# Kernel tuning notes

Hardware: AMD Instinct MI355X
Metric: run time of the kernel (lower is better)

The kernel has to match this reference:

```python
import jax, jax.numpy as jnp
import numpy as np

D_MODEL = 1024
EXPAND = 2
D_INNER = D_MODEL * EXPAND  # 2048
D_STATE = 16
DT_RANK = 64
CONV_K = 4
LN_EPS = 1e-5
B_SZ, SEQ = 2, 2048


def setup_inputs() -> dict:
    key = jax.random.key(0)
    ks = jax.random.split(key, 10)
    x = jax.random.normal(ks[0], (B_SZ, SEQ, D_MODEL), dtype=jnp.float32)
    ln_g = jnp.ones((D_MODEL,), jnp.float32)
    ln_b = jnp.zeros((D_MODEL,), jnp.float32)
    W_in = jax.random.normal(ks[1], (2 * D_INNER, D_MODEL), jnp.float32) * 0.02
    conv_w = jax.random.normal(ks[2], (D_INNER, 1, CONV_K), jnp.float32) * 0.2
    conv_b = jnp.zeros((D_INNER,), jnp.float32)
    # A_log = log(repeat(arange(1..d_state), d_inner))
    A_log = jnp.log(jnp.broadcast_to(jnp.arange(1, D_STATE + 1, dtype=jnp.float32), (D_INNER, D_STATE)))
    D_param = jnp.ones((D_INNER,), jnp.float32)
    x_proj_w = jax.random.normal(ks[3], (DT_RANK + 2 * D_STATE, D_INNER), jnp.float32) * 0.02
    dt_std = DT_RANK ** -0.5
    dt_w = jax.random.uniform(ks[4], (D_INNER, DT_RANK), jnp.float32, -dt_std, dt_std)
    dt = jnp.exp(jax.random.uniform(ks[5], (D_INNER,), jnp.float32) * (np.log(0.1) - np.log(0.001)) + np.log(0.001))
    dt_b = dt + jnp.log(-jnp.expm1(-dt))  # inverse softplus
    W_out = jax.random.normal(ks[6], (D_MODEL, D_INNER), jnp.float32) * 0.02
    return dict(x=x, ln_g=ln_g, ln_b=ln_b, W_in=W_in, conv_w=conv_w, conv_b=conv_b,
                A_log=A_log, D_param=D_param, x_proj_w=x_proj_w, dt_w=dt_w, dt_b=dt_b, W_out=W_out)


def _selective_scan(u, delta, A, B, C):
    # u, delta: (b,l,d); A: (d,n); B, C: (b,l,n)
    deltaA = jnp.exp(delta[..., None] * A[None, None])          # (b,l,d,n)
    dBu = delta[..., None] * B[:, :, None, :] * u[..., None]    # (b,l,d,n)

    def step(s, inp):
        dA_t, dBu_t, C_t = inp          # (b,d,n), (b,d,n), (b,n)
        s = dA_t * s + dBu_t
        y = jnp.einsum('bdn,bn->bd', s, C_t)
        return s, y

    s0 = jnp.zeros((u.shape[0], u.shape[2], A.shape[1]), u.dtype)
    xs = (jnp.moveaxis(deltaA, 1, 0), jnp.moveaxis(dBu, 1, 0), jnp.moveaxis(C, 1, 0))
    _, ys = jax.lax.scan(step, s0, xs)
    return jnp.moveaxis(ys, 0, 1)       # (b,l,d)


def reference(x, ln_g, ln_b, W_in, conv_w, conv_b, A_log, D_param, x_proj_w, dt_w, dt_b, W_out):
    residual = x
    mu = jnp.mean(x, -1, keepdims=True)
    var = jnp.var(x, -1, keepdims=True)
    xn = (x - mu) * jax.lax.rsqrt(var + LN_EPS) * ln_g + ln_b
    xz = xn @ W_in.T                               # (b,l,2*d_inner)
    xc, z = jnp.split(xz, 2, axis=-1)
    # causal depthwise conv1d (left-pad k-1)
    lhs = jnp.swapaxes(xc, 1, 2)                   # (b,d,l)
    conv = jax.lax.conv_general_dilated(
        lhs, conv_w, window_strides=(1,), padding=[(CONV_K - 1, 0)],
        dimension_numbers=('NCH', 'OIH', 'NCH'), feature_group_count=D_INNER)
    conv = conv + conv_b[None, :, None]
    xc = jax.nn.silu(jnp.swapaxes(conv, 1, 2))     # (b,l,d)
    # selective SSM
    x_dbl = xc @ x_proj_w.T
    delta_r, B, C = jnp.split(x_dbl, [DT_RANK, DT_RANK + D_STATE], axis=-1)
    delta = jax.nn.softplus(delta_r @ dt_w.T + dt_b)
    A = -jnp.exp(A_log)
    y = _selective_scan(xc, delta, A, B, C)
    y = y + xc * D_param
    y = y * jax.nn.silu(z)
    out = y @ W_out.T
    return out + residual
```

## Files before the change

### kernel.cpp

```cpp
#include <hip/hip_runtime.h>
#include <hip/hip_bf16.h>
#include <math.h>

typedef __hip_bfloat16 bf16;

#define D_MODEL 1024
#define D_INNER 2048
#define NTOK    4096
#define SEQ     2048
#define BSZ     2
#define DSTATE  16
#define DTRANK  64
#define NCH     64
#define CHLEN   32
#define NPAIR   4096
#define XDS     128

__device__ __forceinline__ float b2f(bf16 v) { return __bfloat162float(v); }
__device__ __forceinline__ bf16  f2b(float v) { return __float2bfloat16(v); }
__device__ __forceinline__ short f2bs(float v) {
    bf16 h = __float2bfloat16(v);
    short s; __builtin_memcpy(&s, &h, 2); return s;
}

typedef __attribute__((ext_vector_type(8))) short short8;
typedef __attribute__((ext_vector_type(4))) float f32x4;

__device__ __forceinline__ void async_copy16(const void* g, void* l) {
    __builtin_amdgcn_global_load_lds(
        (const __attribute__((address_space(1))) unsigned int*)g,
        (__attribute__((address_space(3))) unsigned int*)l,
        16, 0, 0);
}

__global__ void k_prep(const float* __restrict__ x, const float* __restrict__ g,
                       const float* __restrict__ b, bf16* __restrict__ xn,
                       const float* __restrict__ W_in, short* __restrict__ wInb,
                       const float* __restrict__ xpw, short* __restrict__ xpwb,
                       const float* __restrict__ dtw, short* __restrict__ dtwb,
                       float* __restrict__ xdbl) {
    int bid = blockIdx.x;
    int tid = threadIdx.x;
    if (bid < 4096) {
        int t = bid;
        const float* row = x + (size_t)t * D_MODEL;
        float v[4];
        float s = 0.f, q = 0.f;
#pragma unroll
        for (int i = 0; i < 4; ++i) {
            int idx = tid + i * 256;
            v[i] = row[idx];
            s += v[i]; q += v[i] * v[i];
        }
        __shared__ float sh_s[256], sh_q[256];
        sh_s[tid] = s; sh_q[tid] = q;
        __syncthreads();
        for (int o = 128; o > 0; o >>= 1) {
            if (tid < o) { sh_s[tid] += sh_s[tid + o]; sh_q[tid] += sh_q[tid + o]; }
            __syncthreads();
        }
        float mu  = sh_s[0] * (1.f / D_MODEL);
        float var = sh_q[0] * (1.f / D_MODEL) - mu * mu;
        float rs  = rsqrtf(var + 1e-5f);
#pragma unroll
        for (int i = 0; i < 4; ++i) {
            int idx = tid + i * 256;
            float o = (v[i] - mu) * rs * g[idx] + b[idx];
            xn[(size_t)t * D_MODEL + idx] = f2b(o);
        }
    } else if (bid < 8192) {
        int i = (bid - 4096) * 256 + tid;
        float4 v = reinterpret_cast<const float4*>(W_in)[i];
        short4 o;
        o.x = f2bs(v.x); o.y = f2bs(v.y); o.z = f2bs(v.z); o.w = f2bs(v.w);
        reinterpret_cast<short4*>(wInb)[i] = o;
    } else if (bid < 8448) {
        int i = (bid - 8192) * 256 + tid;
        int row = i >> 9;
        short4 o;
        if (row < 96) {
            float4 v = reinterpret_cast<const float4*>(xpw)[i];
            o.x = f2bs(v.x); o.y = f2bs(v.y); o.z = f2bs(v.z); o.w = f2bs(v.w);
        } else { o.x = o.y = o.z = o.w = 0; }
        reinterpret_cast<short4*>(xpwb)[i] = o;
    } else if (bid < 8576) {
        int i = (bid - 8448) * 256 + tid;
        float4 v = reinterpret_cast<const float4*>(dtw)[i];
        short4 o;
        o.x = f2bs(v.x); o.y = f2bs(v.y); o.z = f2bs(v.z); o.w = f2bs(v.w);
        reinterpret_cast<short4*>(dtwb)[i] = o;
    } else {
        int i = (bid - 8576) * 256 + tid;
        reinterpret_cast<float4*>(xdbl)[i] = (float4){0.f, 0.f, 0.f, 0.f};
    }
}

__global__ void k_f2b(const float* __restrict__ in, short* __restrict__ out) {
    int i = blockIdx.x * 256 + threadIdx.x;
    float4 v = reinterpret_cast<const float4*>(in)[i];
    short4 o;
    o.x = f2bs(v.x); o.y = f2bs(v.y); o.z = f2bs(v.z); o.w = f2bs(v.w);
    reinterpret_cast<short4*>(out)[i] = o;
}

__global__ void k_extract_dr(const float* __restrict__ xdbl, short* __restrict__ drb) {
    int i = blockIdx.x * 256 + threadIdx.x;
    int t = i >> 4;
    int jg = (i & 15) * 4;
    float4 v = *reinterpret_cast<const float4*>(&xdbl[(size_t)t * XDS + jg]);
    short4 o;
    o.x = f2bs(v.x); o.y = f2bs(v.y); o.z = f2bs(v.z); o.w = f2bs(v.w);
    *reinterpret_cast<short4*>(&drb[(size_t)t * DTRANK + jg]) = o;
}

#define GBK 32
template<int NT>
__global__ __launch_bounds__(256) void k_gemm_mfma(
    const short* __restrict__ A, const short* __restrict__ Bw,
    int N, int K, int mode,
    float* __restrict__ Cf, bf16* __restrict__ Cz,
    const float* __restrict__ res, float* __restrict__ Cout,
    const float* __restrict__ bias)
{
    constexpr int ABUF = 128 * GBK;
    constexpr int BBUF = NT * GBK;
    constexpr int AF   = (NT == 128) ? 4 : 2;
    __shared__ short As[2 * ABUF];
    __shared__ short Bs[2 * BBUF];
    const int tid  = threadIdx.x;
    const int lane = tid & 63;
    const int wave = tid >> 6;
    const int rowbase = (NT == 128) ? (wave >> 1) * 64 : wave * 32;
    const int colbase = (NT == 128) ? (wave & 1) * 64 : 0;
    const int m0 = blockIdx.y * 128;
    const int n0 = blockIdx.x * NT;
    const int lm = lane & 15;
    const int koff = (((lane >> 4) ^ ((lane >> 1) & 3)) * 8);

    const int srow = tid >> 2;
    const int skc  = (((tid & 3) ^ ((tid >> 3) & 3)) * 8);
    const size_t a_off0 = (size_t)(m0 + srow) * K + skc;
    const size_t a_off1 = (size_t)(m0 + srow + 64) * K + skc;
    const size_t b_off0 = (size_t)(n0 + srow) * K + skc;
    size_t b_off1 = 0;
    if constexpr (NT == 128) b_off1 = (size_t)(n0 + srow + 64) * K + skc;

    f32x4 acc[AF][4];
#pragma unroll
    for (int i = 0; i < AF; ++i)
#pragma unroll
        for (int j = 0; j < 4; ++j)
            acc[i][j] = (f32x4){0.f, 0.f, 0.f, 0.f};

    const int kchunk = K / gridDim.z;
    const int kbeg = blockIdx.z * kchunk;
    const int kend = kbeg + kchunk;

    {
        char* aD = (char*)As + tid * 16;
        char* bD = (char*)Bs + tid * 16;
        async_copy16(A + a_off0 + kbeg, aD);
        async_copy16(A + a_off1 + kbeg, aD + 4096);
        async_copy16(Bw + b_off0 + kbeg, bD);
        if constexpr (NT == 128) async_copy16(Bw + b_off1 + kbeg, bD + 4096);
    }

    int cur = 0;
    for (int k0 = kbeg; k0 < kend; k0 += GBK) {
        __syncthreads();
        int k1 = k0 + GBK;
        if (k1 < kend) {
            int nxt = cur ^ 1;
            char* aD = (char*)As + nxt * (ABUF * 2) + tid * 16;
            char* bD = (char*)Bs + nxt * (BBUF * 2) + tid * 16;
            async_copy16(A + a_off0 + k1, aD);
            async_copy16(A + a_off1 + k1, aD + 4096);
            async_copy16(Bw + b_off0 + k1, bD);
            if constexpr (NT == 128) async_copy16(Bw + b_off1 + k1, bD + 4096);
        }

        const short* Ab = As + cur * ABUF;
        const short* Bb = Bs + cur * BBUF;
        short8 af[AF], bf[4];
#pragma unroll
        for (int t = 0; t < AF; ++t)
            af[t] = *reinterpret_cast<const short8*>(&Ab[(rowbase + t * 16 + lm) * GBK + koff]);
#pragma unroll
        for (int t = 0; t < 4; ++t)
            bf[t] = *reinterpret_cast<const short8*>(&Bb[(colbase + t * 16 + lm) * GBK + koff]);
#pragma unroll
        for (int tm = 0; tm < AF; ++tm)
#pragma unroll
            for (int tn = 0; tn < 4; ++tn)
                acc[tm][tn] = __builtin_amdgcn_mfma_f32_16x16x32_bf16(
                    af[tm], bf[tn], acc[tm][tn], 0, 0, 0);
        cur ^= 1;
    }

    const int rq = (lane >> 4) * 4;
#pragma unroll
    for (int tm = 0; tm < AF; ++tm) {
#pragma unroll
        for (int tn = 0; tn < 4; ++tn) {
            f32x4 v = acc[tm][tn];
            int col = n0 + colbase + tn * 16 + lm;
#pragma unroll
            for (int r = 0; r < 4; ++r) {
                int row = m0 + rowbase + tm * 16 + rq + r;
                float val = v[r];
                if (mode == 0) {
                    if (col < D_INNER) Cf[(size_t)row * D_INNER + col] = val;
                    else               Cz[(size_t)row * D_INNER + (col - D_INNER)] = f2b(val);
                } else if (mode == 1) {
                    Cout[(size_t)row * N + col] = val + res[(size_t)row * N + col];
                } else if (mode == 2) {
                    atomicAdd(&Cf[(size_t)row * N + col], val);
                } else if (mode == 3) {
                    float a = val + bias[col];
                    float sp = (a > 20.f) ? a : log1pf(expf(a));
                    Cf[(size_t)row * N + col] = sp;
                } else {
                    Cf[(size_t)blockIdx.z * 4096 * N + (size_t)row * N + col] = val;
                }
            }
        }
    }
}

template<int BM>
__global__ __launch_bounds__(512, 2) void k_gemm8(
    const short* __restrict__ A, const short* __restrict__ Bw,
    int N, int K, int mode,
    float* __restrict__ Cf, bf16* __restrict__ Cz)
{
    constexpr int WM    = BM / 2;
    constexpr int MQ    = WM / 32;
    constexpr int ATILE = BM * 64;
    constexpr int ABYT  = BM * 128;
    constexpr int BREG  = BM * 256;
    __shared__ short lds[2 * ATILE + 2 * 16384];
    char* ldsc = (char*)lds;
    const int tid  = threadIdx.x;
    const int lane = tid & 63;
    const int wave = tid >> 6;
    const int wr   = wave >> 2;
    const int wc   = wave & 3;
    const int lm   = lane & 15;
    const int q4   = lane >> 4;

    const int gx = gridDim.x;
    int n2 = blockIdx.y * gx + blockIdx.x;
    const int nwg = gx * gridDim.y;
    n2 = (n2 & 7) * (nwg >> 3) + (n2 >> 3);
    const int m0 = (n2 / gx) * BM;
    const int n0 = (n2 % gx) * 256;

    const int r0  = tid >> 3;
    const int ksw = ((tid & 7) ^ (r0 & 7)) << 3;

    const int NTt   = K / 64 / gridDim.z;
    const int kbase = blockIdx.z * NTt;

    const short* gA = A  + (size_t)(m0 + r0) * K + ksw;
    const short* gB = Bw + (size_t)(n0 + r0) * K + ksw;

#define STAGE_A8(h, kt, bb) do {                                             \
        const short* s_ = gA + (size_t)(h) * 128 * K + (size_t)(kt) * 64;    \
        char* d_ = ldsc + (bb) * ABYT + (h) * 16384 + tid * 16;              \
        async_copy16(s_, d_);                                                \
        async_copy16(s_ + (size_t)64 * K, d_ + 8192);                        \
    } while (0)
#define STAGE_B8(h, kt, bb) do {                                             \
        const short* s_ = gB + (size_t)(h) * 128 * K + (size_t)(kt) * 64;    \
        char* d_ = ldsc + BREG + (bb) * 32768 + (h) * 16384 + tid * 16;      \
        async_copy16(s_, d_);                                                \
        async_copy16(s_ + (size_t)64 * K, d_ + 8192);                        \
    } while (0)

    f32x4 acc[2][2][MQ][2];
#pragma unroll
    for (int a = 0; a < 2; ++a)
#pragma unroll
        for (int c = 0; c < 2; ++c)
#pragma unroll
            for (int t = 0; t < MQ; ++t)
#pragma unroll
                for (int u = 0; u < 2; ++u)
                    acc[a][c][t][u] = (f32x4){0.f, 0.f, 0.f, 0.f};

    STAGE_B8(0, kbase + 0, 0); STAGE_B8(1, kbase + 0, 0);
    STAGE_A8(0, kbase + 0, 0);
    if constexpr (BM == 256) STAGE_A8(1, kbase + 0, 0);
    STAGE_B8(0, kbase + 1, 1); STAGE_B8(1, kbase + 1, 1);
    asm volatile("s_waitcnt vmcnt(4)" ::: "memory");
    __builtin_amdgcn_s_barrier();

    short8 af[MQ][2], bf0[2][2], bf1[2][2];

    for (int tt = 0; tt < NTt; ++tt) {
        const int b  = tt & 1;
        const int bn = b ^ 1;
        const short* lA = lds + b * ATILE + wr * (WM * 64);
        const short* lB = lds + BM * 128 + b * 16384 + (wc >> 1) * 8192;
        const bool stA = (tt + 1 < NTt);
        const bool stB = (tt + 2 < NTt);

#pragma unroll
        for (int t = 0; t < MQ; ++t) {
            const int rr = t * 16 + lm;
            const int x8 = rr & 7;
            af[t][0] = *reinterpret_cast<const short8*>(&lA[rr * 64 + ((q4 ^ x8) << 3)]);
            af[t][1] = *reinterpret_cast<const short8*>(&lA[rr * 64 + (((4 + q4) ^ x8) << 3)]);
        }
#pragma unroll
        for (int t = 0; t < 2; ++t) {
            const int rr = (wc & 1) * 64 + t * 16 + lm;
            const int x8 = rr & 7;
            bf0[t][0] = *reinterpret_cast<const short8*>(&lB[rr * 64 + ((q4 ^ x8) << 3)]);
            bf0[t][1] = *reinterpret_cast<const short8*>(&lB[rr * 64 + (((4 + q4) ^ x8) << 3)]);
        }
        if (stA) STAGE_A8(0, kbase + tt + 1, bn);
        __builtin_amdgcn_s_barrier();
        asm volatile("s_waitcnt lgkmcnt(0)" ::: "memory");
        __builtin_amdgcn_s_setprio(1);
#pragma unroll
        for (int t = 0; t < MQ; ++t)
#pragma unroll
            for (int u = 0; u < 2; ++u) {
                acc[0][0][t][u] = __builtin_amdgcn_mfma_f32_16x16x32_bf16(af[t][0], bf0[u][0], acc[0][0][t][u], 0, 0, 0);
                acc[0][0][t][u] = __builtin_amdgcn_mfma_f32_16x16x32_bf16(af[t][1], bf0[u][1], acc[0][0][t][u], 0, 0, 0);
            }
        __builtin_amdgcn_s_setprio(0);
        __builtin_amdgcn_s_barrier();

#pragma unroll
        for (int t = 0; t < 2; ++t) {
            const int rr = (wc & 1) * 64 + 32 + t * 16 + lm;
            const int x8 = rr & 7;
            bf1[t][0] = *reinterpret_cast<const short8*>(&lB[rr * 64 + ((q4 ^ x8) << 3)]);
            bf1[t][1] = *reinterpret_cast<const short8*>(&lB[rr * 64 + (((4 + q4) ^ x8) << 3)]);
        }
        if constexpr (BM == 256) { if (stA) STAGE_A8(1, kbase + tt + 1, bn); }
        __builtin_amdgcn_s_barrier();
        asm volatile("s_waitcnt lgkmcnt(0)" ::: "memory");
        __builtin_amdgcn_s_setprio(1);
#pragma unroll
        for (int t = 0; t < MQ; ++t)
#pragma unroll
            for (int u = 0; u < 2; ++u) {
                acc[0][1][t][u] = __builtin_amdgcn_mfma_f32_16x16x32_bf16(af[t][0], bf1[u][0], acc[0][1][t][u], 0, 0, 0);
                acc[0][1][t][u] = __builtin_amdgcn_mfma_f32_16x16x32_bf16(af[t][1], bf1[u][1], acc[0][1][t][u], 0, 0, 0);
            }
        __builtin_amdgcn_s_setprio(0);
        __builtin_amdgcn_s_barrier();

#pragma unroll
        for (int t = 0; t < MQ; ++t) {
            const int rr = MQ * 16 + t * 16 + lm;
            const int x8 = rr & 7;
            af[t][0] = *reinterpret_cast<const short8*>(&lA[rr * 64 + ((q4 ^ x8) << 3)]);
            af[t][1] = *reinterpret_cast<const short8*>(&lA[rr * 64 + (((4 + q4) ^ x8) << 3)]);
        }
        if (stB) STAGE_B8(0, kbase + tt + 2, b);
        __builtin_amdgcn_s_barrier();
        asm volatile("s_waitcnt lgkmcnt(0)" ::: "memory");
        __builtin_amdgcn_s_setprio(1);
#pragma unroll
        for (int t = 0; t < MQ; ++t)
#pragma unroll
            for (int u = 0; u < 2; ++u) {
                acc[1][1][t][u] = __builtin_amdgcn_mfma_f32_16x16x32_bf16(af[t][0], bf1[u][0], acc[1][1][t][u], 0, 0, 0);
                acc[1][1][t][u] = __builtin_amdgcn_mfma_f32_16x16x32_bf16(af[t][1], bf1[u][1], acc[1][1][t][u], 0, 0, 0);
            }
        __builtin_amdgcn_s_setprio(0);
        __builtin_amdgcn_s_barrier();

        if (stB) {
            STAGE_B8(1, kbase + tt + 2, b);
            asm volatile("s_waitcnt vmcnt(4)" ::: "memory");
        } else if (stA) {
            asm volatile("s_waitcnt vmcnt(0)" ::: "memory");
        }
        __builtin_amdgcn_s_barrier();
        __builtin_amdgcn_s_setprio(1);
#pragma unroll
        for (int t = 0; t < MQ; ++t)
#pragma unroll
            for (int u = 0; u < 2; ++u) {
                acc[1][0][t][u] = __builtin_amdgcn_mfma_f32_16x16x32_bf16(af[t][0], bf0[u][0], acc[1][0][t][u], 0, 0, 0);
                acc[1][0][t][u] = __builtin_amdgcn_mfma_f32_16x16x32_bf16(af[t][1], bf0[u][1], acc[1][0][t][u], 0, 0, 0);
            }
        __builtin_amdgcn_s_setprio(0);
        __builtin_amdgcn_s_barrier();
    }
#undef STAGE_A8
#undef STAGE_B8

    const int rq = (lane >> 4) * 4;
#pragma unroll
    for (int qr = 0; qr < 2; ++qr)
#pragma unroll
    for (int qc = 0; qc < 2; ++qc)
#pragma unroll
    for (int t = 0; t < MQ; ++t)
#pragma unroll
    for (int u = 0; u < 2; ++u) {
        f32x4 v = acc[qr][qc][t][u];
        const int col = n0 + wc * 64 + qc * 32 + u * 16 + lm;
#pragma unroll
        for (int r = 0; r < 4; ++r) {
            const int row = m0 + wr * WM + qr * (WM / 2) + t * 16 + rq + r;
            if (mode == 0) {
                if (col < D_INNER) Cf[(size_t)row * D_INNER + col] = v[r];
                else               Cz[(size_t)row * D_INNER + (col - D_INNER)] = f2b(v[r]);
            } else {
                Cf[(size_t)blockIdx.z * 4096 * N + (size_t)row * N + col] = v[r];
            }
        }
    }
}

__global__ void k_reduce_out(const float* __restrict__ x, const float* __restrict__ P,
                             float* __restrict__ out) {
    int i = blockIdx.x * 256 + threadIdx.x;
    float4 a = reinterpret_cast<const float4*>(x)[i];
    float4 p = reinterpret_cast<const float4*>(P)[i];
    float4 q = reinterpret_cast<const float4*>(P + (size_t)4096 * 1024)[i];
    float4 o;
    o.x = a.x + p.x + q.x; o.y = a.y + p.y + q.y;
    o.z = a.z + p.z + q.z; o.w = a.w + p.w + q.w;
    reinterpret_cast<float4*>(out)[i] = o;
}

__global__ void k_conv(const float* __restrict__ xc, const float* __restrict__ cw,
                       const float* __restrict__ cb, bf16* __restrict__ xcs) {
    size_t idx = (size_t)blockIdx.x * blockDim.x + threadIdx.x;
    int d = (int)(idx & (D_INNER - 1));
    int l = (int)((idx >> 11) & (SEQ - 1));
    float w0 = cw[d * 4 + 0], w1 = cw[d * 4 + 1];
    float w2 = cw[d * 4 + 2], w3 = cw[d * 4 + 3];
    const float* base = xc + idx;
    float acc = cb[d] + w3 * base[0];
    if (l >= 1) acc += w2 * base[-(int)D_INNER];
    if (l >= 2) acc += w1 * base[-2 * (int)D_INNER];
    if (l >= 3) acc += w0 * base[-3 * (int)D_INNER];
    xcs[idx] = f2b(acc / (1.f + __expf(-acc)));
}

__global__ __launch_bounds__(256) void k_scan_partialB(
    const float* __restrict__ delta, const bf16* __restrict__ xcs,
    const float* __restrict__ xdbl, const float* __restrict__ A_log,
    bf16* __restrict__ chs, float* __restrict__ sumdl)
{
    __shared__ float Bsh[CHLEN][16];
    const int tid = threadIdx.x;
    const int d = blockIdx.x * 256 + tid;
    const int chunk = blockIdx.y;
    const int b = blockIdx.z;
    const size_t tbase = (size_t)b * SEQ + (size_t)chunk * CHLEN;

    if (tid < 128) {
        int t = tid >> 2, j = (tid & 3) * 4;
        float4 v = *reinterpret_cast<const float4*>(&xdbl[(tbase + t) * XDS + 64 + j]);
        *reinterpret_cast<float4*>(&Bsh[t][j]) = v;
    }
    float An[16];
#pragma unroll
    for (int j = 0; j < 4; ++j) {
        float4 v = *reinterpret_cast<const float4*>(&A_log[(size_t)d * DSTATE + j * 4]);
        An[j * 4 + 0] = -__expf(v.x); An[j * 4 + 1] = -__expf(v.y);
        An[j * 4 + 2] = -__expf(v.z); An[j * 4 + 3] = -__expf(v.w);
    }
    __syncthreads();

    float s[16];
#pragma unroll
    for (int n = 0; n < 16; ++n) s[n] = 0.f;
    float sd = 0.f;
    for (int t = 0; t < CHLEN; ++t) {
        size_t gt = tbase + t;
        float dl = delta[gt * D_INNER + d];
        float u  = b2f(xcs[gt * D_INNER + d]);
        float dlu = dl * u;
        sd += dl;
#pragma unroll
        for (int n = 0; n < 16; ++n) {
            float dA = __expf(dl * An[n]);
            s[n] = fmaf(dA, s[n], dlu * Bsh[t][n]);
        }
    }
    const int pair = b * D_INNER + d;
    bf16* co = chs + ((size_t)pair * NCH + chunk) * DSTATE;
#pragma unroll
    for (int n = 0; n < 16; ++n) co[n] = f2b(s[n]);
    sumdl[(size_t)pair * NCH + chunk] = sd;
}

__global__ void k_scan_combineB(const bf16* __restrict__ chs, const float* __restrict__ sumdl,
                                const float* __restrict__ A_log, bf16* __restrict__ sst) {
    int idx = blockIdx.x * 256 + threadIdx.x;
    int pair = idx >> 4;
    int n = idx & 15;
    int d = pair & (D_INNER - 1);
    float An = -__expf(A_log[(size_t)d * DSTATE + n]);
    float s = 0.f;
    for (int c = 0; c < NCH; ++c) {
        size_t o = ((size_t)pair * NCH + c) * DSTATE + n;
        float loc = b2f(chs[o]);
        float ap = __expf(An * sumdl[(size_t)pair * NCH + c]);
        sst[o] = f2b(s);
        s = fmaf(ap, s, loc);
    }
}

__global__ __launch_bounds__(256) void k_scan_finalB(
    const float* __restrict__ delta, const bf16* __restrict__ xcs,
    const float* __restrict__ xdbl, const bf16* __restrict__ zbuf,
    const float* __restrict__ A_log, const float* __restrict__ Dp,
    const bf16* __restrict__ sst, bf16* __restrict__ yf)
{
    __shared__ float BC[CHLEN][32];
    const int tid = threadIdx.x;
    const int d = blockIdx.x * 256 + tid;
    const int chunk = blockIdx.y;
    const int b = blockIdx.z;
    const size_t tbase = (size_t)b * SEQ + (size_t)chunk * CHLEN;

    {
        int t = tid >> 3, j = (tid & 7) * 4;
        float4 v = *reinterpret_cast<const float4*>(&xdbl[(tbase + t) * XDS + 64 + j]);
        *reinterpret_cast<float4*>(&BC[t][j]) = v;
    }
    float An[16];
#pragma unroll
    for (int j = 0; j < 4; ++j) {
        float4 v = *reinterpret_cast<const float4*>(&A_log[(size_t)d * DSTATE + j * 4]);
        An[j * 4 + 0] = -__expf(v.x); An[j * 4 + 1] = -__expf(v.y);
        An[j * 4 + 2] = -__expf(v.z); An[j * 4 + 3] = -__expf(v.w);
    }
    const int pair = b * D_INNER + d;
    float s[16];
    const bf16* so = sst + ((size_t)pair * NCH + chunk) * DSTATE;
#pragma unroll
    for (int n = 0; n < 16; ++n) s[n] = b2f(so[n]);
    const float Dv = Dp[d];
    __syncthreads();

    for (int t = 0; t < CHLEN; ++t) {
        size_t gt = tbase + t;
        float dl = delta[gt * D_INNER + d];
        float u  = b2f(xcs[gt * D_INNER + d]);
        float dlu = dl * u;
        float y = 0.f;
#pragma unroll
        for (int n = 0; n < 16; ++n) {
            float dA = __expf(dl * An[n]);
            s[n] = fmaf(dA, s[n], dlu * BC[t][n]);
            y = fmaf(s[n], BC[t][16 + n], y);
        }
        float zv = b2f(zbuf[gt * D_INNER + d]);
        float sz = zv / (1.f + __expf(-zv));
        yf[gt * D_INNER + d] = f2b((y + u * Dv) * sz);
    }
}

extern "C" void kernel_launch(void* const* d_in, const int* in_sizes, int n_in,
                              void* d_out, int out_size, void* d_ws, size_t ws_size,
                              hipStream_t stream) {
    const float* x      = (const float*)d_in[0];
    const float* ln_g   = (const float*)d_in[1];
    const float* ln_b   = (const float*)d_in[2];
    const float* W_in   = (const float*)d_in[3];
    const float* conv_w = (const float*)d_in[4];
    const float* conv_b = (const float*)d_in[5];
    const float* A_log  = (const float*)d_in[6];
    const float* D_par  = (const float*)d_in[7];
    const float* xpw    = (const float*)d_in[8];
    const float* dtw    = (const float*)d_in[9];
    const float* dtb    = (const float*)d_in[10];
    const float* W_out  = (const float*)d_in[11];
    float* out = (float*)d_out;

    char* ws = (char*)d_ws;
    bf16*  xn    = (bf16*)(ws + 0);
    bf16*  chs   = (bf16*)(ws + 0);
    bf16*  sst   = chs;
    short* wOutb = (short*)(ws + 0);
    float* xc    = (float*)(ws + 8388608);
    float* delta = xc;
    float* P0    = (float*)(ws + 8388608);
    bf16*  z     = (bf16*)(ws + 41943040);
    bf16*  yf    = z;
    short* wInb  = (short*)(ws + 58720256);
    bf16*  xcs   = (bf16*)(ws + 58720256);
    float* xdbl  = (float*)(ws + 75497472);
    float* sumdl = (float*)(ws + 77594624);
    short* drb   = (short*)(ws + 78643200);
    short* dtwb  = (short*)(ws + 79167488);
    short* xpwb  = (short*)(ws + 79429632);

    k_prep<<<9088, 256, 0, stream>>>(x, ln_g, ln_b, xn, W_in, wInb, xpw, xpwb, dtw, dtwb, xdbl);
    k_gemm8<256><<<dim3(4096 / 256, 4096 / 256, 1), 512, 0, stream>>>(
        (const short*)xn, wInb, 2 * D_INNER, D_MODEL, 0, xc, z);
    k_conv<<<(NTOK * D_INNER) / 256, 256, 0, stream>>>(xc, conv_w, conv_b, xcs);
    k_gemm_mfma<64><<<dim3(2, 32, 8), 256, 0, stream>>>(
        (const short*)xcs, xpwb, XDS, D_INNER, 2, xdbl, nullptr, nullptr, nullptr, nullptr);
    k_extract_dr<<<(NTOK * DTRANK / 4) / 256, 256, 0, stream>>>(xdbl, drb);
    k_gemm_mfma<64><<<dim3(D_INNER / 64, 32, 1), 256, 0, stream>>>(
        drb, dtwb, D_INNER, DTRANK, 3, delta, nullptr, nullptr, nullptr, dtb);
    k_scan_partialB<<<dim3(D_INNER / 256, NCH, BSZ), 256, 0, stream>>>(
        delta, xcs, xdbl, A_log, chs, sumdl);
    k_scan_combineB<<<(NPAIR * DSTATE) / 256, 256, 0, stream>>>(chs, sumdl, A_log, sst);
    k_scan_finalB<<<dim3(D_INNER / 256, NCH, BSZ), 256, 0, stream>>>(
        delta, xcs, xdbl, z, A_log, D_par, sst, yf);
    k_f2b<<<(D_MODEL * D_INNER / 4) / 256, 256, 0, stream>>>(W_out, wOutb);
    k_gemm8<128><<<dim3(D_MODEL / 256, 4096 / 128, 2), 512, 0, stream>>>(
        (const short*)yf, wOutb, D_MODEL, D_INNER, 4, P0, nullptr);
    k_reduce_out<<<(NTOK * D_MODEL / 4) / 256, 256, 0, stream>>>(x, P0, out);
}
```

Measured before the change: 363.2 us.

## Replace atomic split-K x_proj with partial buffers plus reduction; restructure gemm8 pipeline

The x_proj split-K GEMM now writes eight per-slice partial buffers (mode 4) instead of accumulating into a zeroed xdbl. A new reduction kernel sums the slices and writes both the bf16 dt-rank input and the fp32 B/C columns, which removes the zeroing pass in k_prep and the separate extract kernel. Separately, the 8-wave GEMM main loop is reordered: A and B global-to-LDS stages are issued at the start of each half-iteration, MFMA blocks are merged, and several barriers and lgkmcnt waits are dropped, with sched_barrier added to pin the ordering. Fewer barriers raise the risk of LDS read/write races and add extra traffic for the partial buffers.

```diff
diff --git a/kernel.cpp b/kernel.cpp
--- a/kernel.cpp
+++ b/kernel.cpp
@@ -37,8 +37,7 @@
                        const float* __restrict__ b, bf16* __restrict__ xn,
                        const float* __restrict__ W_in, short* __restrict__ wInb,
                        const float* __restrict__ xpw, short* __restrict__ xpwb,
-                       const float* __restrict__ dtw, short* __restrict__ dtwb,
-                       float* __restrict__ xdbl) {
+                       const float* __restrict__ dtw, short* __restrict__ dtwb) {
     int bid = blockIdx.x;
     int tid = threadIdx.x;
     if (bid < 4096) {
@@ -83,15 +82,12 @@
             o.x = f2bs(v.x); o.y = f2bs(v.y); o.z = f2bs(v.z); o.w = f2bs(v.w);
         } else { o.x = o.y = o.z = o.w = 0; }
         reinterpret_cast<short4*>(xpwb)[i] = o;
-    } else if (bid < 8576) {
+    } else {
         int i = (bid - 8448) * 256 + tid;
         float4 v = reinterpret_cast<const float4*>(dtw)[i];
         short4 o;
         o.x = f2bs(v.x); o.y = f2bs(v.y); o.z = f2bs(v.z); o.w = f2bs(v.w);
         reinterpret_cast<short4*>(dtwb)[i] = o;
-    } else {
-        int i = (bid - 8576) * 256 + tid;
-        reinterpret_cast<float4*>(xdbl)[i] = (float4){0.f, 0.f, 0.f, 0.f};
     }
 }
 
@@ -103,14 +99,25 @@
     reinterpret_cast<short4*>(out)[i] = o;
 }
 
-__global__ void k_extract_dr(const float* __restrict__ xdbl, short* __restrict__ drb) {
+__global__ void k_xproj_red(const float* __restrict__ P, short* __restrict__ drb,
+                            float* __restrict__ xdbl) {
     int i = blockIdx.x * 256 + threadIdx.x;
-    int t = i >> 4;
-    int jg = (i & 15) * 4;
-    float4 v = *reinterpret_cast<const float4*>(&xdbl[(size_t)t * XDS + jg]);
-    short4 o;
-    o.x = f2bs(v.x); o.y = f2bs(v.y); o.z = f2bs(v.z); o.w = f2bs(v.w);
-    *reinterpret_cast<short4*>(&drb[(size_t)t * DTRANK + jg]) = o;
+    int t = i >> 5;
+    int c4 = (i & 31) * 4;
+    const float* p = P + (size_t)t * XDS + c4;
+    float4 s = *reinterpret_cast<const float4*>(p);
+#pragma unroll
+    for (int z = 1; z < 8; ++z) {
+        float4 v = *reinterpret_cast<const float4*>(p + (size_t)z * 4096 * XDS);
+        s.x += v.x; s.y += v.y; s.z += v.z; s.w += v.w;
+    }
+    if (c4 < DTRANK) {
+        short4 o;
+        o.x = f2bs(s.x); o.y = f2bs(s.y); o.z = f2bs(s.z); o.w = f2bs(s.w);
+        *reinterpret_cast<short4*>(&drb[(size_t)t * DTRANK + c4]) = o;
+    } else {
+        *reinterpret_cast<float4*>(&xdbl[(size_t)t * XDS + c4]) = s;
+    }
 }
 
 #define GBK 32
@@ -294,6 +301,7 @@
     STAGE_B8(0, kbase + 1, 1); STAGE_B8(1, kbase + 1, 1);
     asm volatile("s_waitcnt vmcnt(4)" ::: "memory");
     __builtin_amdgcn_s_barrier();
+    __builtin_amdgcn_sched_barrier(0);
 
     short8 af[MQ][2], bf0[2][2], bf1[2][2];
 
@@ -305,6 +313,10 @@
         const bool stA = (tt + 1 < NTt);
         const bool stB = (tt + 2 < NTt);
 
+        if (stA) {
+            STAGE_A8(0, kbase + tt + 1, bn);
+            if constexpr (BM == 256) STAGE_A8(1, kbase + tt + 1, bn);
+        }
 #pragma unroll
         for (int t = 0; t < MQ; ++t) {
             const int rr = t * 16 + lm;
@@ -319,20 +331,6 @@
             bf0[t][0] = *reinterpret_cast<const short8*>(&lB[rr * 64 + ((q4 ^ x8) << 3)]);
             bf0[t][1] = *reinterpret_cast<const short8*>(&lB[rr * 64 + (((4 + q4) ^ x8) << 3)]);
         }
-        if (stA) STAGE_A8(0, kbase + tt + 1, bn);
-        __builtin_amdgcn_s_barrier();
-        asm volatile("s_waitcnt lgkmcnt(0)" ::: "memory");
-        __builtin_amdgcn_s_setprio(1);
-#pragma unroll
-        for (int t = 0; t < MQ; ++t)
-#pragma unroll
-            for (int u = 0; u < 2; ++u) {
-                acc[0][0][t][u] = __builtin_amdgcn_mfma_f32_16x16x32_bf16(af[t][0], bf0[u][0], acc[0][0][t][u], 0, 0, 0);
-                acc[0][0][t][u] = __builtin_amdgcn_mfma_f32_16x16x32_bf16(af[t][1], bf0[u][1], acc[0][0][t][u], 0, 0, 0);
-            }
-        __builtin_amdgcn_s_setprio(0);
-        __builtin_amdgcn_s_barrier();
-
 #pragma unroll
         for (int t = 0; t < 2; ++t) {
             const int rr = (wc & 1) * 64 + 32 + t * 16 + lm;
@@ -340,10 +338,14 @@
             bf1[t][0] = *reinterpret_cast<const short8*>(&lB[rr * 64 + ((q4 ^ x8) << 3)]);
             bf1[t][1] = *reinterpret_cast<const short8*>(&lB[rr * 64 + (((4 + q4) ^ x8) << 3)]);
         }
-        if constexpr (BM == 256) { if (stA) STAGE_A8(1, kbase + tt + 1, bn); }
-        __builtin_amdgcn_s_barrier();
-        asm volatile("s_waitcnt lgkmcnt(0)" ::: "memory");
         __builtin_amdgcn_s_setprio(1);
+#pragma unroll
+        for (int t = 0; t < MQ; ++t)
+#pragma unroll
+            for (int u = 0; u < 2; ++u) {
+                acc[0][0][t][u] = __builtin_amdgcn_mfma_f32_16x16x32_bf16(af[t][0], bf0[u][0], acc[0][0][t][u], 0, 0, 0);
+                acc[0][0][t][u] = __builtin_amdgcn_mfma_f32_16x16x32_bf16(af[t][1], bf0[u][1], acc[0][0][t][u], 0, 0, 0);
+            }
 #pragma unroll
         for (int t = 0; t < MQ; ++t)
 #pragma unroll
@@ -353,7 +355,12 @@
             }
         __builtin_amdgcn_s_setprio(0);
         __builtin_amdgcn_s_barrier();
-
+        __builtin_amdgcn_sched_barrier(0);
+
+        if (stB) {
+            STAGE_B8(0, kbase + tt + 2, b);
+            STAGE_B8(1, kbase + tt + 2, b);
+        }
 #pragma unroll
         for (int t = 0; t < MQ; ++t) {
             const int rr = MQ * 16 + t * 16 + lm;
@@ -361,10 +368,14 @@
             af[t][0] = *reinterpret_cast<const short8*>(&lA[rr * 64 + ((q4 ^ x8) << 3)]);
             af[t][1] = *reinterpret_cast<const short8*>(&lA[rr * 64 + (((4 + q4) ^ x8) << 3)]);
         }
-        if (stB) STAGE_B8(0, kbase + tt + 2, b);
-        __builtin_amdgcn_s_barrier();
-        asm volatile("s_waitcnt lgkmcnt(0)" ::: "memory");
         __builtin_amdgcn_s_setprio(1);
+#pragma unroll
+        for (int t = 0; t < MQ; ++t)
+#pragma unroll
+            for (int u = 0; u < 2; ++u) {
+                acc[1][0][t][u] = __builtin_amdgcn_mfma_f32_16x16x32_bf16(af[t][0], bf0[u][0], acc[1][0][t][u], 0, 0, 0);
+                acc[1][0][t][u] = __builtin_amdgcn_mfma_f32_16x16x32_bf16(af[t][1], bf0[u][1], acc[1][0][t][u], 0, 0, 0);
+            }
 #pragma unroll
         for (int t = 0; t < MQ; ++t)
 #pragma unroll
@@ -373,25 +384,13 @@
                 acc[1][1][t][u] = __builtin_amdgcn_mfma_f32_16x16x32_bf16(af[t][1], bf1[u][1], acc[1][1][t][u], 0, 0, 0);
             }
         __builtin_amdgcn_s_setprio(0);
-        __builtin_amdgcn_s_barrier();
-
         if (stB) {
-            STAGE_B8(1, kbase + tt + 2, b);
             asm volatile("s_waitcnt vmcnt(4)" ::: "memory");
         } else if (stA) {
             asm volatile("s_waitcnt vmcnt(0)" ::: "memory");
         }
         __builtin_amdgcn_s_barrier();
-        __builtin_amdgcn_s_setprio(1);
-#pragma unroll
-        for (int t = 0; t < MQ; ++t)
-#pragma unroll
-            for (int u = 0; u < 2; ++u) {
-                acc[1][0][t][u] = __builtin_amdgcn_mfma_f32_16x16x32_bf16(af[t][0], bf0[u][0], acc[1][0][t][u], 0, 0, 0);
-                acc[1][0][t][u] = __builtin_amdgcn_mfma_f32_16x16x32_bf16(af[t][1], bf0[u][1], acc[1][0][t][u], 0, 0, 0);
-            }
-        __builtin_amdgcn_s_setprio(0);
-        __builtin_amdgcn_s_barrier();
+        __builtin_amdgcn_sched_barrier(0);
     }
 #undef STAGE_A8
 #undef STAGE_B8
@@ -587,6 +586,7 @@
     bf16*  sst   = chs;
     short* wOutb = (short*)(ws + 0);
     float* xc    = (float*)(ws + 8388608);
+    float* Pxp   = (float*)(ws + 8388608);
     float* delta = xc;
     float* P0    = (float*)(ws + 8388608);
     bf16*  z     = (bf16*)(ws + 41943040);
@@ -599,13 +599,13 @@
     short* dtwb  = (short*)(ws + 79167488);
     short* xpwb  = (short*)(ws + 79429632);
 
-    k_prep<<<9088, 256, 0, stream>>>(x, ln_g, ln_b, xn, W_in, wInb, xpw, xpwb, dtw, dtwb, xdbl);
+    k_prep<<<8576, 256, 0, stream>>>(x, ln_g, ln_b, xn, W_in, wInb, xpw, xpwb, dtw, dtwb);
     k_gemm8<256><<<dim3(4096 / 256, 4096 / 256, 1), 512, 0, stream>>>(
         (const short*)xn, wInb, 2 * D_INNER, D_MODEL, 0, xc, z);
     k_conv<<<(NTOK * D_INNER) / 256, 256, 0, stream>>>(xc, conv_w, conv_b, xcs);
     k_gemm_mfma<64><<<dim3(2, 32, 8), 256, 0, stream>>>(
-        (const short*)xcs, xpwb, XDS, D_INNER, 2, xdbl, nullptr, nullptr, nullptr, nullptr);
-    k_extract_dr<<<(NTOK * DTRANK / 4) / 256, 256, 0, stream>>>(xdbl, drb);
+        (const short*)xcs, xpwb, XDS, D_INNER, 4, Pxp, nullptr, nullptr, nullptr, nullptr);
+    k_xproj_red<<<(NTOK * 32) / 256, 256, 0, stream>>>(Pxp, drb, xdbl);
     k_gemm_mfma<64><<<dim3(D_INNER / 64, 32, 1), 256, 0, stream>>>(
         drb, dtwb, D_INNER, DTRANK, 3, delta, nullptr, nullptr, nullptr, dtb);
     k_scan_partialB<<<dim3(D_INNER / 256, NCH, BSZ), 256, 0, stream>>>(
```

New measurement: 350.8 us. 3.4% less time.
